# Kernel optimization log

Measured on AMD Instinct MI355X. Metric: run time of the kernel, lower is better.

Reference implementation:

```python
import jax, jax.numpy as jnp
import numpy as np

CH = 256
NH = 8
HD = CH // NH  # 32


def setup_inputs() -> dict:
    key = jax.random.key(0)
    k1, k2, k3, k4 = jax.random.split(key, 4)
    x = jax.random.normal(k1, (2, CH, 16, 16, 16), dtype=jnp.float32)
    # 1x1x1 Conv3d weights == per-voxel linear maps over channels
    qkv_w = jax.random.normal(k2, (3 * CH, CH), dtype=jnp.float32) * (1.0 / np.sqrt(CH))
    proj_w = jax.random.normal(k3, (CH, CH), dtype=jnp.float32) * (1.0 / np.sqrt(CH))
    proj_b = jax.random.normal(k4, (CH,), dtype=jnp.float32) * 0.01
    return {"x": x, "qkv_w": qkv_w, "proj_w": proj_w, "proj_b": proj_b}


def reference(x, qkv_w, proj_w, proj_b):
    B, C, D, H, W = x.shape
    N = D * H * W
    nh, hd = NH, HD
    xf = x.reshape(B, C, N)  # [B, C, N]
    # qkv 1x1x1 conv: [B, 3C, N]
    qkv = jnp.einsum('oc,bcn->bon', qkv_w, xf)
    # split channel dim as (3, nh, hd), then arrange to [3, B, nh, N, hd]
    qkv = qkv.reshape(B, 3, nh, hd, N).transpose(1, 0, 2, 4, 3)
    q, k, v = qkv[0], qkv[1], qkv[2]
    scale = hd ** -0.5
    attn = jnp.einsum('bhqd,bhkd->bhqk', q, k) * scale  # [B, nh, N, N]
    attn = jax.nn.softmax(attn, axis=-1)
    # dropout is identity in eval mode
    out = jnp.einsum('bhqk,bhkd->bhqd', attn, v)  # [B, nh, N, hd]
    out = out.transpose(0, 1, 3, 2).reshape(B, C, D, H, W)
    out = jnp.einsum('oc,bcdhw->bodhw', proj_w, out) + proj_b[None, :, None, None, None]
    return out
```

## Files before the change

kernel.cpp:

```cpp
#include <hip/hip_runtime.h>
#include <hip/hip_bf16.h>

typedef __bf16 bf16;
typedef __bf16 bf16x8 __attribute__((ext_vector_type(8)));
typedef float f32x4 __attribute__((ext_vector_type(4)));
typedef float f32x16 __attribute__((ext_vector_type(16)));
typedef unsigned int u32x4 __attribute__((ext_vector_type(4)));

#define EXP2(x) __builtin_amdgcn_exp2f(x)

static __device__ __forceinline__ f32x4 mfma16(bf16x8 a, bf16x8 b, f32x4 c) {
    return __builtin_amdgcn_mfma_f32_16x16x32_bf16(a, b, c, 0, 0, 0);
}
static __device__ __forceinline__ f32x16 mfma32(bf16x8 a, bf16x8 b, f32x16 c) {
    return __builtin_amdgcn_mfma_f32_32x32x16_bf16(a, b, c, 0, 0, 0);
}
static __device__ __forceinline__ unsigned cvt_pk(float lo, float hi) {
    unsigned r;
    asm("v_cvt_pk_bf16_f32 %0, %1, %2" : "=v"(r) : "v"(lo), "v"(hi));
    return r;
}
static __device__ __forceinline__ void perm32swap(unsigned &a, unsigned &b) {
    asm("v_permlane32_swap_b32 %0, %1" : "+v"(a), "+v"(b));
}

__global__ __launch_bounds__(256) void prep_w_kernel(const float* __restrict__ qkv_w,
                                                     const float* __restrict__ proj_w,
                                                     bf16* __restrict__ wqkv,
                                                     bf16* __restrict__ Wp) {
    int idx = blockIdx.x * 256 + threadIdx.x;
    const float QSCALE = 0.17677669529663689f * 1.4426950408889634f;
    if (idx < 768 * 256) {
        float v = qkv_w[idx];
        if (idx < 256 * 256) v *= QSCALE;
        wqkv[idx] = (bf16)v;
    } else {
        int j = idx - 768 * 256;
        int o = j >> 8, c = j & 255;
        int ot = o >> 5, l31 = o & 31;
        int kc = c >> 4, hi = (c >> 3) & 1, jj = c & 7;
        Wp[(size_t)(((ot * 16 + kc) * 64 + hi * 32 + l31) * 8 + jj)] = (bf16)proj_w[j];
    }
}

__global__ __launch_bounds__(256) void transpose_x_kernel(const float* __restrict__ x,
                                                          bf16* __restrict__ xT) {
    __shared__ float tile[64][68];
    int b = blockIdx.z, cb = blockIdx.y * 64, nb = blockIdx.x * 64;
    int t = threadIdx.x;
    int j = t & 15, rc = t >> 4;
    const float* src = x + ((size_t)b * 256 + cb) * 4096 + nb;
#pragma unroll
    for (int i = 0; i < 4; i++) {
        f32x4 v = *(const f32x4*)(src + (size_t)(rc + i * 16) * 4096 + j * 4);
        *(f32x4*)&tile[rc + i * 16][j * 4] = v;
    }
    __syncthreads();
    int n = t >> 2;
    bf16* dst = xT + ((size_t)b * 4096 + nb + n) * 256 + cb;
#pragma unroll
    for (int i = 0; i < 2; i++) {
        int c0 = ((t & 3) + i * 4) * 8;
        bf16x8 v;
#pragma unroll
        for (int jj = 0; jj < 8; jj++) v[jj] = (bf16)tile[c0 + jj][n];
        *(bf16x8*)(dst + c0) = v;
    }
}

__global__ __launch_bounds__(256) void qkv_gemm_kernel(const bf16* __restrict__ xT,
                                                       const bf16* __restrict__ w,
                                                       bf16* __restrict__ Q,
                                                       bf16* __restrict__ Kp,
                                                       bf16* __restrict__ Vp) {
    int b = blockIdx.z;
    int nb = blockIdx.x * 64, ob = blockIdx.y * 128;
    int t = threadIdx.x, wid = t >> 6, lane = t & 63;
    int l15 = lane & 15, g = lane >> 4;
    int wr = wid >> 1, wc = wid & 1;
    const bf16* xrow = xT + ((size_t)b * 4096 + nb + wr * 32 + l15) * 256 + g * 8;
    const bf16* wrow = w + (size_t)(ob + wc * 64 + l15) * 256 + g * 8;
    f32x4 acc[2][4] = {};
    for (int k0 = 0; k0 < 256; k0 += 32) {
        bf16x8 a[2], bb[4];
#pragma unroll
        for (int rt = 0; rt < 2; rt++) a[rt] = *(const bf16x8*)(xrow + rt * 16 * 256 + k0);
#pragma unroll
        for (int cg = 0; cg < 4; cg++) bb[cg] = *(const bf16x8*)(wrow + cg * 16 * 256 + k0);
#pragma unroll
        for (int rt = 0; rt < 2; rt++)
#pragma unroll
            for (int cg = 0; cg < 4; cg++)
                acc[rt][cg] = mfma16(a[rt], bb[cg], acc[rt][cg]);
    }
#pragma unroll
    for (int rt = 0; rt < 2; rt++) {
#pragma unroll
        for (int cg = 0; cg < 4; cg++) {
            int o = ob + wc * 64 + cg * 16 + l15;
            int tsel = o >> 8;
            int h = (o >> 5) & 7;
            int d = o & 31;
            int n0 = nb + wr * 32 + rt * 16 + g * 4;
            size_t bhbase = ((size_t)b * 8 + h) * 131072;
            if (tsel == 0) {
#pragma unroll
                for (int i = 0; i < 4; i++)
                    Q[(((size_t)b * 8 + h) * 4096 + n0 + i) * 32 + d] = (bf16)acc[rt][cg][i];
            } else if (tsel == 1) {
                int kt = n0 >> 5;
                int which = d >> 4, hi2 = (d >> 3) & 1, j = d & 7;
                size_t base = bhbase + (size_t)(((kt * 2 + which) * 64 + hi2 * 32) * 8 + j);
#pragma unroll
                for (int i = 0; i < 4; i++) {
                    int r5 = (n0 + i) & 31;
                    Kp[base + r5 * 8] = (bf16)acc[rt][cg][i];
                }
            } else {
                int kt = n0 >> 5, kk0 = n0 & 31;
                int which = kk0 >> 4, hi2 = (kk0 >> 3) & 1, j0 = kk0 & 7;
                unsigned p0 = cvt_pk(acc[rt][cg][0], acc[rt][cg][1]);
                unsigned p1 = cvt_pk(acc[rt][cg][2], acc[rt][cg][3]);
                uint2 wv; wv.x = p0; wv.y = p1;
                *(uint2*)(Vp + bhbase + (size_t)(((kt * 2 + which) * 64 + hi2 * 32 + d) * 8 + j0)) = wv;
            }
        }
    }
}

#define PACK(stv, B, OUT) {                                  \
    unsigned _x01 = cvt_pk(stv[B + 0], stv[B + 1]);          \
    unsigned _x23 = cvt_pk(stv[B + 2], stv[B + 3]);          \
    unsigned _y01 = cvt_pk(stv[B + 4], stv[B + 5]);          \
    unsigned _y23 = cvt_pk(stv[B + 6], stv[B + 7]);          \
    perm32swap(_x01, _y01);                                  \
    perm32swap(_x23, _y23);                                  \
    u32x4 _w = {_x01, _x23, _y01, _y23};                     \
    OUT = __builtin_bit_cast(bf16x8, _w); }

#define PROC(ST, OACC, LP) {                                 \
    _Pragma("unroll")                                        \
    for (int r = 0; r < 16; r++) ST[r] = EXP2(ST[r]);        \
    float _s0 = 0.f, _s1 = 0.f;                              \
    _Pragma("unroll")                                        \
    for (int r = 0; r < 8; r++) { _s0 += ST[r]; _s1 += ST[r + 8]; } \
    LP += _s0 + _s1;                                         \
    bf16x8 _pb0, _pb1;                                       \
    PACK(ST, 0, _pb0);                                       \
    PACK(ST, 8, _pb1);                                       \
    __builtin_amdgcn_s_setprio(1);                           \
    OACC = mfma32(vf0, _pb0, OACC);                          \
    OACC = mfma32(vf1, _pb1, OACC);                          \
    __builtin_amdgcn_s_setprio(0); }

__global__ __launch_bounds__(256) void attn_kernel(const bf16* __restrict__ Q,
                                                   const bf16* __restrict__ Kp,
                                                   const bf16* __restrict__ Vp,
                                                   bf16* __restrict__ attP) {
    __shared__ __align__(16) float ldsO[3][2][64][20];
    __shared__ float ldsL[3][2][32];

    const int w = blockIdx.x;
    const int bh = (w & 7) + 8 * ((w >> 3) & 1);
    const int qblk = w >> 4;
    const int t = threadIdx.x;
    const int z = t >> 6, lane = t & 63;
    const int l31 = lane & 31, hi = lane >> 5;
    const int q0 = qblk * 64;

    const bf16* __restrict__ Qb = Q + (size_t)bh * 4096 * 32;
    const bf16* kptr = Kp + (size_t)bh * 131072 + (size_t)z * 32768 + lane * 8;
    const bf16* vptr = Vp + (size_t)bh * 131072 + (size_t)z * 32768 + lane * 8;

    bf16x8 qfA0 = *(const bf16x8*)(Qb + (size_t)(q0 + l31) * 32 + hi * 8);
    bf16x8 qfA1 = *(const bf16x8*)(Qb + (size_t)(q0 + l31) * 32 + 16 + hi * 8);
    bf16x8 qfB0 = *(const bf16x8*)(Qb + (size_t)(q0 + 32 + l31) * 32 + hi * 8);
    bf16x8 qfB1 = *(const bf16x8*)(Qb + (size_t)(q0 + 32 + l31) * 32 + 16 + hi * 8);

    const f32x16 ZERO16 = {};
    f32x16 oA = {}, oB = {};
    float lA = 0.f, lB = 0.f;

    for (int it = 0; it < 32; ++it) {
        bf16x8 kf0 = *(const bf16x8*)(kptr);
        bf16x8 kf1 = *(const bf16x8*)(kptr + 512);
        bf16x8 vf0 = *(const bf16x8*)(vptr);
        bf16x8 vf1 = *(const bf16x8*)(vptr + 512);
        kptr += 1024; vptr += 1024;

        f32x16 st = mfma32(kf0, qfA0, ZERO16);
        st = mfma32(kf1, qfA1, st);
        PROC(st, oA, lA);
        st = mfma32(kf0, qfB0, ZERO16);
        st = mfma32(kf1, qfB1, st);
        PROC(st, oB, lB);
    }

    lA += __shfl_xor(lA, 32);
    lB += __shfl_xor(lB, 32);

    if (z != 0) {
#pragma unroll
        for (int g = 0; g < 4; g++) {
            *(f32x4*)&ldsO[z - 1][0][lane][4 * g] =
                f32x4{oA[4 * g + 0], oA[4 * g + 1], oA[4 * g + 2], oA[4 * g + 3]};
            *(f32x4*)&ldsO[z - 1][1][lane][4 * g] =
                f32x4{oB[4 * g + 0], oB[4 * g + 1], oB[4 * g + 2], oB[4 * g + 3]};
        }
        if (hi == 0) { ldsL[z - 1][0][l31] = lA; ldsL[z - 1][1][l31] = lB; }
    }
    __syncthreads();
    if (z == 0) {
        const int b = bh >> 3, h = bh & 7;
#pragma unroll
        for (int qg = 0; qg < 2; qg++) {
            const f32x16& oo = qg ? oB : oA;
            float lsum = (qg ? lB : lA) + ldsL[0][qg][l31] + ldsL[1][qg][l31] + ldsL[2][qg][l31];
            float inv = __builtin_amdgcn_rcpf(lsum);
            int nt = qblk * 2 + qg;
            size_t base = (((size_t)b * 128 + nt) * 16) * 512;
#pragma unroll
            for (int g = 0; g < 4; g++) {
                f32x4 p0 = *(const f32x4*)&ldsO[0][qg][lane][4 * g];
                f32x4 p1 = *(const f32x4*)&ldsO[1][qg][lane][4 * g];
                f32x4 p2 = *(const f32x4*)&ldsO[2][qg][lane][4 * g];
                float e0 = (oo[4 * g + 0] + p0[0] + p1[0] + p2[0]) * inv;
                float e1 = (oo[4 * g + 1] + p0[1] + p1[1] + p2[1]) * inv;
                float e2 = (oo[4 * g + 2] + p0[2] + p1[2] + p2[2]) * inv;
                float e3 = (oo[4 * g + 3] + p0[3] + p1[3] + p2[3]) * inv;
                size_t addr = base + (size_t)(((h * 2 + (g >> 1)) * 64 + (g & 1) * 32 + l31) * 8 + 4 * hi);
                uint2 wv;
                wv.x = cvt_pk(e0, e1);
                wv.y = cvt_pk(e2, e3);
                *(uint2*)(attP + addr) = wv;
            }
        }
    }
}

__global__ __launch_bounds__(256) void proj_gemm_kernel(const bf16* __restrict__ attP,
                                                        const bf16* __restrict__ Wp,
                                                        const float* __restrict__ bias,
                                                        float* __restrict__ out) {
    int bid = blockIdx.x;
    int b = bid >> 8, rest = bid & 255;
    int nt = rest >> 1, oh = rest & 1;
    int t = threadIdx.x, wid = t >> 6, lane = t & 63;
    int l31 = lane & 31, hi = lane >> 5;
    int ot = oh * 4 + wid;

    const bf16* ap = Wp + (size_t)(ot * 16) * 512 + lane * 8;
    const bf16* bp = attP + (((size_t)b * 128 + nt) * 16) * 512 + lane * 8;
    f32x16 acc = {};
#pragma unroll
    for (int kc = 0; kc < 16; kc++) {
        bf16x8 af = *(const bf16x8*)(ap + kc * 512);
        bf16x8 bf = *(const bf16x8*)(bp + kc * 512);
        acc = mfma32(af, bf, acc);
    }
    float* obase = out + ((size_t)b * 256 + ot * 32) * 4096 + nt * 32 + l31;
#pragma unroll
    for (int r = 0; r < 16; r++) {
        int row = (r & 3) + 8 * (r >> 2) + 4 * hi;
        obase[(size_t)row * 4096] = acc[r] + bias[ot * 32 + row];
    }
}

extern "C" void kernel_launch(void* const* d_in, const int* in_sizes, int n_in,
                              void* d_out, int out_size, void* d_ws, size_t ws_size,
                              hipStream_t stream) {
    const float* x      = (const float*)d_in[0];
    const float* qkv_w  = (const float*)d_in[1];
    const float* proj_w = (const float*)d_in[2];
    const float* proj_b = (const float*)d_in[3];
    float* out = (float*)d_out;

    char* ws = (char*)d_ws;
    bf16* xT    = (bf16*)(ws);
    bf16* wqkv  = (bf16*)(ws + 4194304);
    bf16* Wp    = (bf16*)(ws + 4587520);
    bf16* Qb    = (bf16*)(ws + 4718592);
    bf16* Kp    = (bf16*)(ws + 8912896);
    bf16* Vp    = (bf16*)(ws + 13107200);
    bf16* attP  = (bf16*)(ws + 17301504);

    prep_w_kernel<<<1024, 256, 0, stream>>>(qkv_w, proj_w, wqkv, Wp);
    transpose_x_kernel<<<dim3(64, 4, 2), 256, 0, stream>>>(x, xT);
    qkv_gemm_kernel<<<dim3(64, 6, 2), 256, 0, stream>>>(xT, wqkv, Qb, Kp, Vp);
    attn_kernel<<<1024, 256, 0, stream>>>(Qb, Kp, Vp, attP);
    proj_gemm_kernel<<<512, 256, 0, stream>>>(attP, Wp, proj_b, out);
}
```

Baseline: 99.74 us.

## Split attention query block across 8 waves with staggered key start offsets

```diff
diff --git a/kernel.cpp b/kernel.cpp
--- a/kernel.cpp
+++ b/kernel.cpp
@@ -138,25 +138,36 @@
     u32x4 _w = {_x01, _x23, _y01, _y23};                     \
     OUT = __builtin_bit_cast(bf16x8, _w); }
 
-#define PROC(ST, OACC, LP) {                                 \
-    _Pragma("unroll")                                        \
-    for (int r = 0; r < 16; r++) ST[r] = EXP2(ST[r]);        \
-    float _s0 = 0.f, _s1 = 0.f;                              \
-    _Pragma("unroll")                                        \
-    for (int r = 0; r < 8; r++) { _s0 += ST[r]; _s1 += ST[r + 8]; } \
-    LP += _s0 + _s1;                                         \
-    bf16x8 _pb0, _pb1;                                       \
-    PACK(ST, 0, _pb0);                                       \
-    PACK(ST, 8, _pb1);                                       \
-    __builtin_amdgcn_s_setprio(1);                           \
-    OACC = mfma32(vf0, _pb0, OACC);                          \
-    OACC = mfma32(vf1, _pb1, OACC);                          \
-    __builtin_amdgcn_s_setprio(0); }
-
-__global__ __launch_bounds__(256) void attn_kernel(const bf16* __restrict__ Q,
-                                                   const bf16* __restrict__ Kp,
-                                                   const bf16* __restrict__ Vp,
-                                                   bf16* __restrict__ attP) {
+#define SEG(KP, VP, CNT) {                                   \
+    const bf16* _kp = (KP);                                  \
+    const bf16* _vp = (VP);                                  \
+    for (int _i = 0; _i < (CNT); ++_i) {                     \
+        bf16x8 kf0 = *(const bf16x8*)(_kp);                  \
+        bf16x8 kf1 = *(const bf16x8*)(_kp + 512);            \
+        bf16x8 vf0 = *(const bf16x8*)(_vp);                  \
+        bf16x8 vf1 = *(const bf16x8*)(_vp + 512);            \
+        _kp += 1024; _vp += 1024;                            \
+        f32x16 st = mfma32(kf0, qf0, ZERO16);                \
+        st = mfma32(kf1, qf1, st);                           \
+        _Pragma("unroll")                                    \
+        for (int r = 0; r < 16; r++) st[r] = EXP2(st[r]);    \
+        float _s0 = 0.f, _s1 = 0.f;                          \
+        _Pragma("unroll")                                    \
+        for (int r = 0; r < 8; r++) { _s0 += st[r]; _s1 += st[r + 8]; } \
+        lpart += _s0 + _s1;                                  \
+        bf16x8 _pb0, _pb1;                                   \
+        PACK(st, 0, _pb0);                                   \
+        PACK(st, 8, _pb1);                                   \
+        __builtin_amdgcn_s_setprio(1);                       \
+        o_acc = mfma32(vf0, _pb0, o_acc);                    \
+        o_acc = mfma32(vf1, _pb1, o_acc);                    \
+        __builtin_amdgcn_s_setprio(0);                       \
+    } }
+
+__global__ __launch_bounds__(512, 6) void attn_kernel(const bf16* __restrict__ Q,
+                                                      const bf16* __restrict__ Kp,
+                                                      const bf16* __restrict__ Vp,
+                                                      bf16* __restrict__ attP) {
     __shared__ __align__(16) float ldsO[3][2][64][20];
     __shared__ float ldsL[3][2][32];
 
@@ -164,76 +175,57 @@
     const int bh = (w & 7) + 8 * ((w >> 3) & 1);
     const int qblk = w >> 4;
     const int t = threadIdx.x;
-    const int z = t >> 6, lane = t & 63;
+    const int wid = t >> 6, lane = t & 63;
+    const int zraw = wid >> 1, wq = wid & 1;
+    const int z = (zraw + qblk) & 3;
     const int l31 = lane & 31, hi = lane >> 5;
-    const int q0 = qblk * 64;
+    const int q0 = qblk * 64 + wq * 32;
 
     const bf16* __restrict__ Qb = Q + (size_t)bh * 4096 * 32;
-    const bf16* kptr = Kp + (size_t)bh * 131072 + (size_t)z * 32768 + lane * 8;
-    const bf16* vptr = Vp + (size_t)bh * 131072 + (size_t)z * 32768 + lane * 8;
-
-    bf16x8 qfA0 = *(const bf16x8*)(Qb + (size_t)(q0 + l31) * 32 + hi * 8);
-    bf16x8 qfA1 = *(const bf16x8*)(Qb + (size_t)(q0 + l31) * 32 + 16 + hi * 8);
-    bf16x8 qfB0 = *(const bf16x8*)(Qb + (size_t)(q0 + 32 + l31) * 32 + hi * 8);
-    bf16x8 qfB1 = *(const bf16x8*)(Qb + (size_t)(q0 + 32 + l31) * 32 + 16 + hi * 8);
+    const bf16* kq = Kp + (size_t)bh * 131072 + (size_t)z * 32768 + lane * 8;
+    const bf16* vq = Vp + (size_t)bh * 131072 + (size_t)z * 32768 + lane * 8;
+
+    bf16x8 qf0 = *(const bf16x8*)(Qb + (size_t)(q0 + l31) * 32 + hi * 8);
+    bf16x8 qf1 = *(const bf16x8*)(Qb + (size_t)(q0 + l31) * 32 + 16 + hi * 8);
 
     const f32x16 ZERO16 = {};
-    f32x16 oA = {}, oB = {};
-    float lA = 0.f, lB = 0.f;
-
-    for (int it = 0; it < 32; ++it) {
-        bf16x8 kf0 = *(const bf16x8*)(kptr);
-        bf16x8 kf1 = *(const bf16x8*)(kptr + 512);
-        bf16x8 vf0 = *(const bf16x8*)(vptr);
-        bf16x8 vf1 = *(const bf16x8*)(vptr + 512);
-        kptr += 1024; vptr += 1024;
-
-        f32x16 st = mfma32(kf0, qfA0, ZERO16);
-        st = mfma32(kf1, qfA1, st);
-        PROC(st, oA, lA);
-        st = mfma32(kf0, qfB0, ZERO16);
-        st = mfma32(kf1, qfB1, st);
-        PROC(st, oB, lB);
-    }
-
-    lA += __shfl_xor(lA, 32);
-    lB += __shfl_xor(lB, 32);
-
-    if (z != 0) {
+    f32x16 o_acc = {};
+    float lpart = 0.f;
+
+    const int st0 = (qblk * 11) & 31;
+    SEG(kq + (size_t)st0 * 1024, vq + (size_t)st0 * 1024, 32 - st0);
+    SEG(kq, vq, st0);
+
+    lpart += __shfl_xor(lpart, 32);
+
+    if (zraw != 0) {
+#pragma unroll
+        for (int g = 0; g < 4; g++)
+            *(f32x4*)&ldsO[zraw - 1][wq][lane][4 * g] =
+                f32x4{o_acc[4 * g + 0], o_acc[4 * g + 1], o_acc[4 * g + 2], o_acc[4 * g + 3]};
+        if (hi == 0) ldsL[zraw - 1][wq][l31] = lpart;
+    }
+    __syncthreads();
+    if (zraw == 0) {
+        const int b = bh >> 3, h = bh & 7;
+        float lsum = lpart + ldsL[0][wq][l31] + ldsL[1][wq][l31] + ldsL[2][wq][l31];
+        float inv = __builtin_amdgcn_rcpf(lsum);
+        int nt = qblk * 2 + wq;
+        size_t base = (((size_t)b * 128 + nt) * 16) * 512;
 #pragma unroll
         for (int g = 0; g < 4; g++) {
-            *(f32x4*)&ldsO[z - 1][0][lane][4 * g] =
-                f32x4{oA[4 * g + 0], oA[4 * g + 1], oA[4 * g + 2], oA[4 * g + 3]};
-            *(f32x4*)&ldsO[z - 1][1][lane][4 * g] =
-                f32x4{oB[4 * g + 0], oB[4 * g + 1], oB[4 * g + 2], oB[4 * g + 3]};
-        }
-        if (hi == 0) { ldsL[z - 1][0][l31] = lA; ldsL[z - 1][1][l31] = lB; }
-    }
-    __syncthreads();
-    if (z == 0) {
-        const int b = bh >> 3, h = bh & 7;
-#pragma unroll
-        for (int qg = 0; qg < 2; qg++) {
-            const f32x16& oo = qg ? oB : oA;
-            float lsum = (qg ? lB : lA) + ldsL[0][qg][l31] + ldsL[1][qg][l31] + ldsL[2][qg][l31];
-            float inv = __builtin_amdgcn_rcpf(lsum);
-            int nt = qblk * 2 + qg;
-            size_t base = (((size_t)b * 128 + nt) * 16) * 512;
-#pragma unroll
-            for (int g = 0; g < 4; g++) {
-                f32x4 p0 = *(const f32x4*)&ldsO[0][qg][lane][4 * g];
-                f32x4 p1 = *(const f32x4*)&ldsO[1][qg][lane][4 * g];
-                f32x4 p2 = *(const f32x4*)&ldsO[2][qg][lane][4 * g];
-                float e0 = (oo[4 * g + 0] + p0[0] + p1[0] + p2[0]) * inv;
-                float e1 = (oo[4 * g + 1] + p0[1] + p1[1] + p2[1]) * inv;
-                float e2 = (oo[4 * g + 2] + p0[2] + p1[2] + p2[2]) * inv;
-                float e3 = (oo[4 * g + 3] + p0[3] + p1[3] + p2[3]) * inv;
-                size_t addr = base + (size_t)(((h * 2 + (g >> 1)) * 64 + (g & 1) * 32 + l31) * 8 + 4 * hi);
-                uint2 wv;
-                wv.x = cvt_pk(e0, e1);
-                wv.y = cvt_pk(e2, e3);
-                *(uint2*)(attP + addr) = wv;
-            }
+            f32x4 p0 = *(const f32x4*)&ldsO[0][wq][lane][4 * g];
+            f32x4 p1 = *(const f32x4*)&ldsO[1][wq][lane][4 * g];
+            f32x4 p2 = *(const f32x4*)&ldsO[2][wq][lane][4 * g];
+            float e0 = (o_acc[4 * g + 0] + p0[0] + p1[0] + p2[0]) * inv;
+            float e1 = (o_acc[4 * g + 1] + p0[1] + p1[1] + p2[1]) * inv;
+            float e2 = (o_acc[4 * g + 2] + p0[2] + p1[2] + p2[2]) * inv;
+            float e3 = (o_acc[4 * g + 3] + p0[3] + p1[3] + p2[3]) * inv;
+            size_t addr = base + (size_t)(((h * 2 + (g >> 1)) * 64 + (g & 1) * 32 + l31) * 8 + 4 * hi);
+            uint2 wv;
+            wv.x = cvt_pk(e0, e1);
+            wv.y = cvt_pk(e2, e3);
+            *(uint2*)(attP + addr) = wv;
         }
     }
 }
@@ -287,6 +279,6 @@
     prep_w_kernel<<<1024, 256, 0, stream>>>(qkv_w, proj_w, wqkv, Wp);
     transpose_x_kernel<<<dim3(64, 4, 2), 256, 0, stream>>>(x, xT);
     qkv_gemm_kernel<<<dim3(64, 6, 2), 256, 0, stream>>>(xT, wqkv, Qb, Kp, Vp);
-    attn_kernel<<<1024, 256, 0, stream>>>(Qb, Kp, Vp, attP);
+    attn_kernel<<<1024, 512, 0, stream>>>(Qb, Kp, Vp, attP);
     proj_gemm_kernel<<<512, 256, 0, stream>>>(attP, Wp, proj_b, out);
 }
```

New measurement: 90.57 us. 1.1x faster.

## Split attention key range across eight waves per block with staggered start

Applied to the files above, without the earlier changes.

```diff
diff --git a/kernel.cpp b/kernel.cpp
--- a/kernel.cpp
+++ b/kernel.cpp
@@ -153,24 +153,25 @@
     OACC = mfma32(vf1, _pb1, OACC);                          \
     __builtin_amdgcn_s_setprio(0); }
 
-__global__ __launch_bounds__(256) void attn_kernel(const bf16* __restrict__ Q,
-                                                   const bf16* __restrict__ Kp,
-                                                   const bf16* __restrict__ Vp,
-                                                   bf16* __restrict__ attP) {
-    __shared__ __align__(16) float ldsO[3][2][64][20];
-    __shared__ float ldsL[3][2][32];
+__global__ __launch_bounds__(512, 4) void attn_kernel(const bf16* __restrict__ Q,
+                                                      const bf16* __restrict__ Kp,
+                                                      const bf16* __restrict__ Vp,
+                                                      bf16* __restrict__ attP) {
+    __shared__ __align__(16) float ldsO[7][2][64][20];
+    __shared__ float ldsL[7][2][32];
 
     const int w = blockIdx.x;
     const int bh = (w & 7) + 8 * ((w >> 3) & 1);
     const int qblk = w >> 4;
     const int t = threadIdx.x;
-    const int z = t >> 6, lane = t & 63;
+    const int zraw = t >> 6, lane = t & 63;
+    const int z = (zraw + qblk) & 7;
     const int l31 = lane & 31, hi = lane >> 5;
     const int q0 = qblk * 64;
 
-    const bf16* __restrict__ Qb = Q + (size_t)bh * 4096 * 32;
-    const bf16* kptr = Kp + (size_t)bh * 131072 + (size_t)z * 32768 + lane * 8;
-    const bf16* vptr = Vp + (size_t)bh * 131072 + (size_t)z * 32768 + lane * 8;
+    const bf16* __restrict__ Qb = Q + (size_t)bh * 131072;
+    const bf16* kp = Kp + (size_t)bh * 131072 + (size_t)z * 16384 + lane * 8;
+    const bf16* vp = Vp + (size_t)bh * 131072 + (size_t)z * 16384 + lane * 8;
 
     bf16x8 qfA0 = *(const bf16x8*)(Qb + (size_t)(q0 + l31) * 32 + hi * 8);
     bf16x8 qfA1 = *(const bf16x8*)(Qb + (size_t)(q0 + l31) * 32 + 16 + hi * 8);
@@ -179,55 +180,58 @@
 
     const f32x16 ZERO16 = {};
     f32x16 oA = {}, oB = {};
-    float lA = 0.f, lB = 0.f;
-
-    for (int it = 0; it < 32; ++it) {
-        bf16x8 kf0 = *(const bf16x8*)(kptr);
-        bf16x8 kf1 = *(const bf16x8*)(kptr + 512);
-        bf16x8 vf0 = *(const bf16x8*)(vptr);
-        bf16x8 vf1 = *(const bf16x8*)(vptr + 512);
-        kptr += 1024; vptr += 1024;
+    float lpA = 0.f, lpB = 0.f;
+
+    for (int it = 0; it < 16; ++it) {
+        bf16x8 kf0 = *(const bf16x8*)(kp);
+        bf16x8 kf1 = *(const bf16x8*)(kp + 512);
+        bf16x8 vf0 = *(const bf16x8*)(vp);
+        bf16x8 vf1 = *(const bf16x8*)(vp + 512);
+        kp += 1024; vp += 1024;
 
         f32x16 st = mfma32(kf0, qfA0, ZERO16);
         st = mfma32(kf1, qfA1, st);
-        PROC(st, oA, lA);
+        PROC(st, oA, lpA);
         st = mfma32(kf0, qfB0, ZERO16);
         st = mfma32(kf1, qfB1, st);
-        PROC(st, oB, lB);
-    }
-
-    lA += __shfl_xor(lA, 32);
-    lB += __shfl_xor(lB, 32);
-
-    if (z != 0) {
+        PROC(st, oB, lpB);
+    }
+
+    lpA += __shfl_xor(lpA, 32);
+    lpB += __shfl_xor(lpB, 32);
+
+    if (zraw != 0) {
 #pragma unroll
         for (int g = 0; g < 4; g++) {
-            *(f32x4*)&ldsO[z - 1][0][lane][4 * g] =
+            *(f32x4*)&ldsO[zraw - 1][0][lane][4 * g] =
                 f32x4{oA[4 * g + 0], oA[4 * g + 1], oA[4 * g + 2], oA[4 * g + 3]};
-            *(f32x4*)&ldsO[z - 1][1][lane][4 * g] =
+            *(f32x4*)&ldsO[zraw - 1][1][lane][4 * g] =
                 f32x4{oB[4 * g + 0], oB[4 * g + 1], oB[4 * g + 2], oB[4 * g + 3]};
         }
-        if (hi == 0) { ldsL[z - 1][0][l31] = lA; ldsL[z - 1][1][l31] = lB; }
+        if (hi == 0) { ldsL[zraw - 1][0][l31] = lpA; ldsL[zraw - 1][1][l31] = lpB; }
     }
     __syncthreads();
-    if (z == 0) {
+    if (zraw == 0) {
         const int b = bh >> 3, h = bh & 7;
 #pragma unroll
         for (int qg = 0; qg < 2; qg++) {
             const f32x16& oo = qg ? oB : oA;
-            float lsum = (qg ? lB : lA) + ldsL[0][qg][l31] + ldsL[1][qg][l31] + ldsL[2][qg][l31];
+            float lsum = qg ? lpB : lpA;
+#pragma unroll
+            for (int s = 0; s < 7; s++) lsum += ldsL[s][qg][l31];
             float inv = __builtin_amdgcn_rcpf(lsum);
             int nt = qblk * 2 + qg;
             size_t base = (((size_t)b * 128 + nt) * 16) * 512;
 #pragma unroll
             for (int g = 0; g < 4; g++) {
-                f32x4 p0 = *(const f32x4*)&ldsO[0][qg][lane][4 * g];
-                f32x4 p1 = *(const f32x4*)&ldsO[1][qg][lane][4 * g];
-                f32x4 p2 = *(const f32x4*)&ldsO[2][qg][lane][4 * g];
-                float e0 = (oo[4 * g + 0] + p0[0] + p1[0] + p2[0]) * inv;
-                float e1 = (oo[4 * g + 1] + p0[1] + p1[1] + p2[1]) * inv;
-                float e2 = (oo[4 * g + 2] + p0[2] + p1[2] + p2[2]) * inv;
-                float e3 = (oo[4 * g + 3] + p0[3] + p1[3] + p2[3]) * inv;
+                float e0 = oo[4 * g + 0], e1 = oo[4 * g + 1];
+                float e2 = oo[4 * g + 2], e3 = oo[4 * g + 3];
+#pragma unroll
+                for (int s = 0; s < 7; s++) {
+                    f32x4 p = *(const f32x4*)&ldsO[s][qg][lane][4 * g];
+                    e0 += p[0]; e1 += p[1]; e2 += p[2]; e3 += p[3];
+                }
+                e0 *= inv; e1 *= inv; e2 *= inv; e3 *= inv;
                 size_t addr = base + (size_t)(((h * 2 + (g >> 1)) * 64 + (g & 1) * 32 + l31) * 8 + 4 * hi);
                 uint2 wv;
                 wv.x = cvt_pk(e0, e1);
@@ -287,6 +291,6 @@
     prep_w_kernel<<<1024, 256, 0, stream>>>(qkv_w, proj_w, wqkv, Wp);
     transpose_x_kernel<<<dim3(64, 4, 2), 256, 0, stream>>>(x, xT);
     qkv_gemm_kernel<<<dim3(64, 6, 2), 256, 0, stream>>>(xT, wqkv, Qb, Kp, Vp);
-    attn_kernel<<<1024, 256, 0, stream>>>(Qb, Kp, Vp, attP);
+    attn_kernel<<<1024, 512, 0, stream>>>(Qb, Kp, Vp, attP);
     proj_gemm_kernel<<<512, 256, 0, stream>>>(attP, Wp, proj_b, out);
 }
```

New measurement: 87.41 us. 12.4% less time.
